# Optimization experiments

Measured on AMD Instinct MI355X. Metric: run time of the kernel, lower is better.

The kernel has to match this reference:

```python
import jax, jax.numpy as jnp
import numpy as np

I, H = 512, 1024

def setup_inputs() -> dict:
    key = jax.random.key(0)
    ks = jax.random.split(key, 5)
    s_ih = 1.0 / np.sqrt(I)
    s_hh = 1.0 / np.sqrt(H)
    return {
        "x": jax.random.normal(ks[0], (512, 64, I), dtype=jnp.float32),
        "W_ih": jax.random.uniform(ks[1], (4 * H, I), minval=-s_ih, maxval=s_ih, dtype=jnp.float32),
        "b_ih": jax.random.uniform(ks[2], (4 * H,), minval=-s_ih, maxval=s_ih, dtype=jnp.float32),
        "W_hh": jax.random.uniform(ks[3], (4 * H, H), minval=-s_hh, maxval=s_hh, dtype=jnp.float32),
        "b_hh": jax.random.uniform(ks[4], (4 * H,), minval=-s_hh, maxval=s_hh, dtype=jnp.float32),
    }

def _lstm(x, W_ih, b_ih, W_hh, b_hh):
    T, B, _ = x.shape
    Hh = W_hh.shape[1]
    # Precompute input projection for all timesteps: [T, B, 4H]
    x_proj = jnp.einsum("tbi,gi->tbg", x, W_ih) + b_ih + b_hh

    def step(carry, xp):
        h, c = carry
        gates = xp + h @ W_hh.T  # [B, 4H]
        i_g, f_g, g_g, o_g = jnp.split(gates, 4, axis=1)
        i_g = jax.nn.sigmoid(i_g)
        f_g = jax.nn.sigmoid(f_g)
        g_g = jnp.tanh(g_g)
        o_g = jax.nn.sigmoid(o_g)
        c = f_g * c + i_g * g_g
        h = o_g * jnp.tanh(c)
        return (h, c), h

    h0 = jnp.zeros((B, Hh), dtype=x.dtype)
    c0 = jnp.zeros((B, Hh), dtype=x.dtype)
    (hT, cT), out = jax.lax.scan(step, (h0, c0), x_proj)
    return out, (hT, cT)

def reference(x, W_ih, b_ih, W_hh, b_hh):
    out, (hT, cT) = _lstm(x, W_ih, b_ih, W_hh, b_hh)
    return out, hT, cT
```

## Files before the change

kernel.cpp:

```cpp
#include <hip/hip_runtime.h>

#define T_STEPS 512
#define BATCH   64
#define IN      512
#define HID     1024
#define GDIM    4096
#define MROWS   (T_STEPS * BATCH)

typedef __attribute__((ext_vector_type(8))) short bf16x8_t;
typedef __attribute__((ext_vector_type(4))) float f32x4_t;

__device__ __forceinline__ unsigned short f2bf(float f) {
  union { float f; unsigned int u; } v; v.f = f;
  unsigned int r = v.u + 0x7FFFu + ((v.u >> 16) & 1u);
  return (unsigned short)(r >> 16);
}
__device__ __forceinline__ float bf2f(unsigned short u) {
  union { unsigned int u; float f; } v; v.u = ((unsigned int)u) << 16;
  return v.f;
}
__device__ __forceinline__ float sigmoidf_(float x) {
  return 1.0f / (1.0f + __expf(-x));
}
__device__ __forceinline__ float tanhf_(float x) {
  return 1.0f - 2.0f / (__expf(2.0f * x) + 1.0f);
}

__global__ void k_cvt(const float* __restrict__ src, unsigned short* __restrict__ dst, int n) {
  int i = (blockIdx.x * blockDim.x + threadIdx.x) * 4;
  if (i + 3 < n) {
    float4 f = *(const float4*)(src + i);
    ushort4 o;
    o.x = f2bf(f.x); o.y = f2bf(f.y); o.z = f2bf(f.z); o.w = f2bf(f.w);
    *(ushort4*)(dst + i) = o;
  }
}

__global__ void k_bias(const float* __restrict__ a, const float* __restrict__ b,
                       float* __restrict__ o) {
  int i = blockIdx.x * blockDim.x + threadIdx.x;
  if (i < GDIM) o[i] = a[i] + b[i];
}

__global__ __launch_bounds__(256) void k_xproj(
    const float* __restrict__ x,
    const unsigned short* __restrict__ Wih,
    const float* __restrict__ bias,
    unsigned short* __restrict__ xproj)
{
  const int AP = 40;
  __shared__ unsigned short Alds[128 * AP];
  __shared__ unsigned short Blds[128 * AP];
  const int tid = threadIdx.x;
  const int w = tid >> 6, l = tid & 63;
  const int m0 = blockIdx.y * 128, n0 = blockIdx.x * 128;
  const int wm = (w >> 1) * 64, wn = (w & 1) * 64;
  f32x4_t acc[4][4] = {};

  for (int k0 = 0; k0 < IN; k0 += 32) {
    #pragma unroll
    for (int it = 0; it < 2; ++it) {
      int chunk = tid + it * 256;
      int row = chunk >> 2;
      int kc  = (chunk & 3) * 8;
      const float* src = x + (size_t)(m0 + row) * IN + k0 + kc;
      float4 f0 = *(const float4*)(src);
      float4 f1 = *(const float4*)(src + 4);
      union { bf16x8_t v; unsigned short s[8]; } u;
      u.s[0]=f2bf(f0.x); u.s[1]=f2bf(f0.y); u.s[2]=f2bf(f0.z); u.s[3]=f2bf(f0.w);
      u.s[4]=f2bf(f1.x); u.s[5]=f2bf(f1.y); u.s[6]=f2bf(f1.z); u.s[7]=f2bf(f1.w);
      *(bf16x8_t*)&Alds[row * AP + kc] = u.v;
    }
    #pragma unroll
    for (int it = 0; it < 2; ++it) {
      int chunk = tid + it * 256;
      int row = chunk >> 2;
      int kc  = (chunk & 3) * 8;
      *(bf16x8_t*)&Blds[row * AP + kc] =
          *(const bf16x8_t*)(Wih + (size_t)(n0 + row) * IN + k0 + kc);
    }
    __syncthreads();
    bf16x8_t a[4], b[4];
    #pragma unroll
    for (int i = 0; i < 4; ++i)
      a[i] = *(const bf16x8_t*)&Alds[(wm + i * 16 + (l & 15)) * AP + ((l >> 4) * 8)];
    #pragma unroll
    for (int i = 0; i < 4; ++i)
      b[i] = *(const bf16x8_t*)&Blds[(wn + i * 16 + (l & 15)) * AP + ((l >> 4) * 8)];
    #pragma unroll
    for (int mi = 0; mi < 4; ++mi) {
      #pragma unroll
      for (int ni = 0; ni < 4; ++ni)
        acc[mi][ni] = __builtin_amdgcn_mfma_f32_16x16x32_bf16(a[mi], b[ni], acc[mi][ni], 0, 0, 0);
    }
    __syncthreads();
  }
  #pragma unroll
  for (int ni = 0; ni < 4; ++ni) {
    int col = n0 + wn + ni * 16 + (l & 15);
    float bv = bias[col];
    #pragma unroll
    for (int mi = 0; mi < 4; ++mi) {
      int rbase = m0 + wm + mi * 16 + (l >> 4) * 4;
      #pragma unroll
      for (int r = 0; r < 4; ++r)
        xproj[(size_t)(rbase + r) * GDIM + col] = f2bf(acc[mi][ni][r] + bv);
    }
  }
}

__global__ __launch_bounds__(256, 1) void k_lstm_persist(
    const unsigned short* __restrict__ xproj,
    const unsigned short* __restrict__ Whh,
    unsigned short* __restrict__ hbuf0,
    unsigned short* __restrict__ hbuf1,
    float* __restrict__ out,
    float* __restrict__ hT,
    float* __restrict__ cT,
    unsigned int* __restrict__ bar)
{
  __shared__ __align__(16) unsigned short Hlds[16384];
  __shared__ float Glds[4][16][17];

  const int tid = threadIdx.x;
  const int w = tid >> 6, l = tid & 63;
  const int bg = blockIdx.x >> 6;
  const int cs = blockIdx.x & 63;
  const int b0 = bg * 16, n0 = cs * 16;

  const int gc = (w << 10) + n0 + (l & 15);
  const unsigned short* wp = Whh + (size_t)gc * HID + ((l >> 4) * 8);
  bf16x8_t wfrag[32];
  #pragma unroll
  for (int ks = 0; ks < 32; ++ks)
    wfrag[ks] = *(const bf16x8_t*)(wp + ks * 32);

  const int eb = tid >> 4, en = tid & 15;
  const size_t ci = (size_t)(b0 + eb) * HID + n0 + en;
  float creg = 0.0f;

  const int abase = (l & 15) * 2048 + ((l >> 4) * 16);
  const int amask = (l & 7) << 4;

  unsigned int* const myflag_base = bar + bg * 512;

  #pragma unroll 1
  for (int t = 0; t < T_STEPS; ++t) {
    const unsigned short* hc = (t & 1) ? hbuf1 : hbuf0;
    unsigned short*       hn = (t & 1) ? hbuf0 : hbuf1;

    const unsigned short* xpp = xproj + ((size_t)t * BATCH + b0 + eb) * GDIM + n0 + en;
    unsigned short x0 = xpp[0], x1 = xpp[1024], x2 = xpp[2048], x3 = xpp[3072];
    asm volatile("" ::: "memory");

    if (t > 0) {
      if (tid == 0) {
        const unsigned int* f = myflag_base + (t - 1);
        while (__hip_atomic_load(f, __ATOMIC_RELAXED, __HIP_MEMORY_SCOPE_AGENT) < 64u)
          __builtin_amdgcn_s_sleep(1);
      }
      __syncthreads();
    }

    {
      const char* hsrc = (const char*)(hc + (size_t)b0 * HID);
      bf16x8_t hv8[8];
      #pragma unroll
      for (int i = 0; i < 8; ++i) {
        unsigned long long ap = (unsigned long long)(hsrc + (size_t)(i * 256 + tid) * 16);
        asm volatile("global_load_dwordx4 %0, %1, off sc0 sc1"
                     : "=v"(hv8[i]) : "v"(ap) : "memory");
      }
      asm volatile("s_waitcnt vmcnt(0)" ::: "memory");
      __builtin_amdgcn_sched_barrier(0);
      #pragma unroll
      for (int i = 0; i < 8; ++i) {
        int d = (i * 256 + tid) * 16;
        int sd = d ^ (((d >> 11) & 7) << 4);
        *(bf16x8_t*)((char*)Hlds + sd) = hv8[i];
      }
    }
    __syncthreads();

    f32x4_t ac0 = {0,0,0,0}, ac1 = {0,0,0,0}, ac2 = {0,0,0,0}, ac3 = {0,0,0,0};
    #pragma unroll
    for (int ks = 0; ks < 32; ks += 4) {
      bf16x8_t a0 = *(const bf16x8_t*)((const char*)Hlds + ((abase + (ks+0)*64) ^ amask));
      bf16x8_t a1 = *(const bf16x8_t*)((const char*)Hlds + ((abase + (ks+1)*64) ^ amask));
      bf16x8_t a2 = *(const bf16x8_t*)((const char*)Hlds + ((abase + (ks+2)*64) ^ amask));
      bf16x8_t a3 = *(const bf16x8_t*)((const char*)Hlds + ((abase + (ks+3)*64) ^ amask));
      ac0 = __builtin_amdgcn_mfma_f32_16x16x32_bf16(a0, wfrag[ks+0], ac0, 0, 0, 0);
      ac1 = __builtin_amdgcn_mfma_f32_16x16x32_bf16(a1, wfrag[ks+1], ac1, 0, 0, 0);
      ac2 = __builtin_amdgcn_mfma_f32_16x16x32_bf16(a2, wfrag[ks+2], ac2, 0, 0, 0);
      ac3 = __builtin_amdgcn_mfma_f32_16x16x32_bf16(a3, wfrag[ks+3], ac3, 0, 0, 0);
    }
    f32x4_t s = ac0 + ac1 + ac2 + ac3;

    {
      int r0 = (l >> 4) * 4, cc = l & 15;
      Glds[w][r0 + 0][cc] = s[0];
      Glds[w][r0 + 1][cc] = s[1];
      Glds[w][r0 + 2][cc] = s[2];
      Glds[w][r0 + 3][cc] = s[3];
    }
    __syncthreads();

    float pre0 = Glds[0][eb][en] + bf2f(x0);
    float pre1 = Glds[1][eb][en] + bf2f(x1);
    float pre2 = Glds[2][eb][en] + bf2f(x2);
    float pre3 = Glds[3][eb][en] + bf2f(x3);
    float ig = sigmoidf_(pre0);
    float fg = sigmoidf_(pre1);
    float gg = tanhf_(pre2);
    float og = sigmoidf_(pre3);
    creg = fg * creg + ig * gg;
    float hv = og * tanhf_(creg);

    out[((size_t)t * BATCH + b0 + eb) * HID + n0 + en] = hv;

    if (t == T_STEPS - 1) {
      hT[ci] = hv;
      cT[ci] = creg;
    } else {
      unsigned short mybf = f2bf(hv);
      unsigned short pbf = (unsigned short)(unsigned int)__shfl_xor((int)(unsigned int)mybf, 1, 64);
      if ((en & 1) == 0) {
        unsigned int pk = ((unsigned int)mybf) | (((unsigned int)pbf) << 16);
        __hip_atomic_store((unsigned int*)(hn + ci), pk,
                           __ATOMIC_RELAXED, __HIP_MEMORY_SCOPE_AGENT);
      }
      asm volatile("s_waitcnt vmcnt(0)" ::: "memory");
      __syncthreads();
      if (tid == 0)
        __hip_atomic_fetch_add(myflag_base + t, 1u,
                               __ATOMIC_RELAXED, __HIP_MEMORY_SCOPE_AGENT);
    }
  }
}

__global__ __launch_bounds__(256) void k_step_fused(
    const unsigned short* __restrict__ hprev,
    unsigned short* __restrict__ hnext,
    float* __restrict__ cstate,
    const unsigned short* __restrict__ Whh,
    const unsigned short* __restrict__ Wih,
    const float* __restrict__ x,
    const float* __restrict__ bias,
    float* __restrict__ out,
    float* __restrict__ hT, float* __restrict__ cT,
    int t, int is_last)
{
  const int RS = 1560;
  const int XB = 1032;
  __shared__ unsigned short Hlds[16 * RS];
  __shared__ float Glds[4][16][17];
  const int tid = threadIdx.x;
  const int w = tid >> 6, l = tid & 63;
  const int bg = blockIdx.x >> 6, hs = blockIdx.x & 63;
  const int b0 = bg * 16, n0 = hs * 16;

  #pragma unroll
  for (int it = 0; it < 8; ++it) {
    int chunk = tid + it * 256;
    int row = chunk >> 7;
    int cc  = (chunk & 127) * 8;
    *(bf16x8_t*)&Hlds[row * RS + cc] =
        *(const bf16x8_t*)(hprev + (size_t)(b0 + row) * HID + cc);
  }
  #pragma unroll
  for (int it = 0; it < 4; ++it) {
    int chunk = tid + it * 256;
    int row = chunk >> 6;
    int cc  = (chunk & 63) * 8;
    const float* src = x + ((size_t)t * BATCH + b0 + row) * IN + cc;
    float4 f0 = *(const float4*)(src);
    float4 f1 = *(const float4*)(src + 4);
    union { bf16x8_t v; unsigned short s[8]; } u;
    u.s[0]=f2bf(f0.x); u.s[1]=f2bf(f0.y); u.s[2]=f2bf(f0.z); u.s[3]=f2bf(f0.w);
    u.s[4]=f2bf(f1.x); u.s[5]=f2bf(f1.y); u.s[6]=f2bf(f1.z); u.s[7]=f2bf(f1.w);
    *(bf16x8_t*)&Hlds[row * RS + XB + cc] = u.v;
  }
  __syncthreads();

  f32x4_t acc = {0.f, 0.f, 0.f, 0.f};
  const int gcol = (w << 10) + n0 + (l & 15);
  const unsigned short* wp = Whh + (size_t)gcol * HID + ((l >> 4) * 8);
  const unsigned short* ap = &Hlds[(l & 15) * RS + ((l >> 4) * 8)];
  #pragma unroll 4
  for (int ks = 0; ks < 32; ++ks) {
    bf16x8_t a = *(const bf16x8_t*)(ap);
    bf16x8_t b = *(const bf16x8_t*)(wp);
    acc = __builtin_amdgcn_mfma_f32_16x16x32_bf16(a, b, acc, 0, 0, 0);
    ap += 32; wp += 32;
  }
  const unsigned short* wpx = Wih + (size_t)gcol * IN + ((l >> 4) * 8);
  const unsigned short* apx = &Hlds[(l & 15) * RS + XB + ((l >> 4) * 8)];
  #pragma unroll 4
  for (int ks = 0; ks < 16; ++ks) {
    bf16x8_t a = *(const bf16x8_t*)(apx);
    bf16x8_t b = *(const bf16x8_t*)(wpx);
    acc = __builtin_amdgcn_mfma_f32_16x16x32_bf16(a, b, acc, 0, 0, 0);
    apx += 32; wpx += 32;
  }

  {
    int r0 = (l >> 4) * 4, cc = l & 15;
    Glds[w][r0 + 0][cc] = acc[0];
    Glds[w][r0 + 1][cc] = acc[1];
    Glds[w][r0 + 2][cc] = acc[2];
    Glds[w][r0 + 3][cc] = acc[3];
  }
  __syncthreads();

  int b = tid >> 4, n = tid & 15;
  float pre[4];
  #pragma unroll
  for (int g = 0; g < 4; ++g)
    pre[g] = Glds[g][b][n] + bias[(g << 10) + n0 + n];
  float ig = sigmoidf_(pre[0]);
  float fg = sigmoidf_(pre[1]);
  float gg = tanhf_(pre[2]);
  float og = sigmoidf_(pre[3]);
  size_t ci = (size_t)(b0 + b) * HID + n0 + n;
  float cn = fg * cstate[ci] + ig * gg;
  float hv = og * tanhf_(cn);
  cstate[ci] = cn;
  out[((size_t)t * BATCH + b0 + b) * HID + n0 + n] = hv;
  hnext[ci] = f2bf(hv);
  if (is_last) { hT[ci] = hv; cT[ci] = cn; }
}

extern "C" void kernel_launch(void* const* d_in, const int* in_sizes, int n_in,
                              void* d_out, int out_size, void* d_ws, size_t ws_size,
                              hipStream_t stream) {
  const float* x    = (const float*)d_in[0];
  const float* Wihf = (const float*)d_in[1];
  const float* bih  = (const float*)d_in[2];
  const float* Whhf = (const float*)d_in[3];
  const float* bhh  = (const float*)d_in[4];
  float* out = (float*)d_out;

  char* ws = (char*)d_ws;
  size_t off = 0;
  auto take = [&](size_t bytes) {
    char* p = ws + off;
    off = (off + bytes + 255) & ~(size_t)255;
    return p;
  };
  unsigned short* wih_b = (unsigned short*)take((size_t)GDIM * IN * 2);
  unsigned short* whh_b = (unsigned short*)take((size_t)GDIM * HID * 2);
  float*          bias  = (float*)take((size_t)GDIM * 4);
  unsigned short* h0    = (unsigned short*)take((size_t)BATCH * HID * 2);
  unsigned short* h1    = (unsigned short*)take((size_t)BATCH * HID * 2);
  float*          cbuf  = (float*)take((size_t)BATCH * HID * 4);
  unsigned int*   bar   = (unsigned int*)take((size_t)T_STEPS * 4 * 4);
  unsigned short* xproj = (unsigned short*)take((size_t)MROWS * GDIM * 2);
  size_t full_need = off;
  const int primary = (ws_size >= full_need) ? 1 : 0;
  (void)in_sizes; (void)n_in; (void)out_size;

  k_cvt<<<(GDIM * IN / 4 + 255) / 256, 256, 0, stream>>>(Wihf, wih_b, GDIM * IN);
  k_cvt<<<(GDIM * HID / 4 + 255) / 256, 256, 0, stream>>>(Whhf, whh_b, GDIM * HID);
  k_bias<<<(GDIM + 255) / 256, 256, 0, stream>>>(bih, bhh, bias);
  (void)hipMemsetAsync(h0, 0, (size_t)BATCH * HID * 2, stream);

  float* hT = out + (size_t)T_STEPS * BATCH * HID;
  float* cT = hT + (size_t)BATCH * HID;

  if (primary) {
    (void)hipMemsetAsync(bar, 0, (size_t)T_STEPS * 4 * 4, stream);
    k_xproj<<<dim3(GDIM / 128, MROWS / 128), 256, 0, stream>>>(x, wih_b, bias, xproj);
    void* args[8];
    void* p_xproj = (void*)xproj; void* p_whh = (void*)whh_b;
    void* p_h0 = (void*)h0;       void* p_h1 = (void*)h1;
    void* p_out = (void*)out;     void* p_hT = (void*)hT;
    void* p_cT = (void*)cT;       void* p_bar = (void*)bar;
    args[0] = &p_xproj; args[1] = &p_whh; args[2] = &p_h0; args[3] = &p_h1;
    args[4] = &p_out;   args[5] = &p_hT;  args[6] = &p_cT; args[7] = &p_bar;
    (void)hipLaunchCooperativeKernel((const void*)k_lstm_persist,
                                     dim3(256), dim3(256), args, 0, stream);
  } else {
    (void)hipMemsetAsync(cbuf, 0, (size_t)BATCH * HID * 4, stream);
    unsigned short* hp = h0;
    unsigned short* hn = h1;
    for (int t = 0; t < T_STEPS; ++t) {
      int last = (t == T_STEPS - 1) ? 1 : 0;
      k_step_fused<<<256, 256, 0, stream>>>(hp, hn, cbuf, whh_b, wih_b, x, bias,
                                            out, hT, cT, t, last);
      unsigned short* tmp = hp; hp = hn; hn = tmp;
    }
  }
}
```

Baseline: 2.083 ms.

## Fuse input projection into persistent LSTM kernel and use per-block flags

Removes the separate x-projection GEMM and its large bf16 workspace. Each persistent block now computes its slice of the next step's input projection right after publishing h, overlapping it with the wait for other blocks. The grid changes from 256 blocks of 256 threads to 128 blocks of 512 threads, so each block owns 32 hidden columns. The atomic counter barrier is replaced by per-block monotonic step flags that a whole wavefront polls with __all. This adds W_ih global reads and MFMA work to the serial recurrence loop, which could lengthen each step if it is not hidden behind the barrier wait.

```diff
diff --git a/kernel.cpp b/kernel.cpp
--- a/kernel.cpp
+++ b/kernel.cpp
@@ -5,7 +5,6 @@
 #define IN      512
 #define HID     1024
 #define GDIM    4096
-#define MROWS   (T_STEPS * BATCH)
 
 typedef __attribute__((ext_vector_type(8))) short bf16x8_t;
 typedef __attribute__((ext_vector_type(4))) float f32x4_t;
@@ -42,142 +41,120 @@
   if (i < GDIM) o[i] = a[i] + b[i];
 }
 
-__global__ __launch_bounds__(256) void k_xproj(
+__global__ __launch_bounds__(512, 1) void k_lstm_persist(
     const float* __restrict__ x,
     const unsigned short* __restrict__ Wih,
-    const float* __restrict__ bias,
-    unsigned short* __restrict__ xproj)
-{
-  const int AP = 40;
-  __shared__ unsigned short Alds[128 * AP];
-  __shared__ unsigned short Blds[128 * AP];
-  const int tid = threadIdx.x;
-  const int w = tid >> 6, l = tid & 63;
-  const int m0 = blockIdx.y * 128, n0 = blockIdx.x * 128;
-  const int wm = (w >> 1) * 64, wn = (w & 1) * 64;
-  f32x4_t acc[4][4] = {};
-
-  for (int k0 = 0; k0 < IN; k0 += 32) {
-    #pragma unroll
-    for (int it = 0; it < 2; ++it) {
-      int chunk = tid + it * 256;
-      int row = chunk >> 2;
-      int kc  = (chunk & 3) * 8;
-      const float* src = x + (size_t)(m0 + row) * IN + k0 + kc;
-      float4 f0 = *(const float4*)(src);
-      float4 f1 = *(const float4*)(src + 4);
-      union { bf16x8_t v; unsigned short s[8]; } u;
-      u.s[0]=f2bf(f0.x); u.s[1]=f2bf(f0.y); u.s[2]=f2bf(f0.z); u.s[3]=f2bf(f0.w);
-      u.s[4]=f2bf(f1.x); u.s[5]=f2bf(f1.y); u.s[6]=f2bf(f1.z); u.s[7]=f2bf(f1.w);
-      *(bf16x8_t*)&Alds[row * AP + kc] = u.v;
-    }
-    #pragma unroll
-    for (int it = 0; it < 2; ++it) {
-      int chunk = tid + it * 256;
-      int row = chunk >> 2;
-      int kc  = (chunk & 3) * 8;
-      *(bf16x8_t*)&Blds[row * AP + kc] =
-          *(const bf16x8_t*)(Wih + (size_t)(n0 + row) * IN + k0 + kc);
-    }
-    __syncthreads();
-    bf16x8_t a[4], b[4];
-    #pragma unroll
-    for (int i = 0; i < 4; ++i)
-      a[i] = *(const bf16x8_t*)&Alds[(wm + i * 16 + (l & 15)) * AP + ((l >> 4) * 8)];
-    #pragma unroll
-    for (int i = 0; i < 4; ++i)
-      b[i] = *(const bf16x8_t*)&Blds[(wn + i * 16 + (l & 15)) * AP + ((l >> 4) * 8)];
-    #pragma unroll
-    for (int mi = 0; mi < 4; ++mi) {
-      #pragma unroll
-      for (int ni = 0; ni < 4; ++ni)
-        acc[mi][ni] = __builtin_amdgcn_mfma_f32_16x16x32_bf16(a[mi], b[ni], acc[mi][ni], 0, 0, 0);
-    }
-    __syncthreads();
-  }
-  #pragma unroll
-  for (int ni = 0; ni < 4; ++ni) {
-    int col = n0 + wn + ni * 16 + (l & 15);
-    float bv = bias[col];
-    #pragma unroll
-    for (int mi = 0; mi < 4; ++mi) {
-      int rbase = m0 + wm + mi * 16 + (l >> 4) * 4;
-      #pragma unroll
-      for (int r = 0; r < 4; ++r)
-        xproj[(size_t)(rbase + r) * GDIM + col] = f2bf(acc[mi][ni][r] + bv);
-    }
-  }
-}
-
-__global__ __launch_bounds__(256, 1) void k_lstm_persist(
-    const unsigned short* __restrict__ xproj,
     const unsigned short* __restrict__ Whh,
+    const float* __restrict__ bih,
+    const float* __restrict__ bhh,
     unsigned short* __restrict__ hbuf0,
     unsigned short* __restrict__ hbuf1,
     float* __restrict__ out,
     float* __restrict__ hT,
     float* __restrict__ cT,
-    unsigned int* __restrict__ bar)
+    unsigned int* __restrict__ flags)
 {
-  __shared__ __align__(16) unsigned short Hlds[16384];
-  __shared__ float Glds[4][16][17];
+  __shared__ __align__(16) unsigned short Hlds[16 * 1024];
+  __shared__ __align__(16) unsigned short Xlds[16 * 512];
+  __shared__ float Glds[4][16][34];
+  __shared__ float XGlds[4][16][34];
 
   const int tid = threadIdx.x;
   const int w = tid >> 6, l = tid & 63;
-  const int bg = blockIdx.x >> 6;
-  const int cs = blockIdx.x & 63;
-  const int b0 = bg * 16, n0 = cs * 16;
-
-  const int gc = (w << 10) + n0 + (l & 15);
+  const int bg  = blockIdx.x >> 5;
+  const int cso = blockIdx.x & 31;
+  const int b0 = bg * 16, n0 = cso * 32;
+  const int g = w & 3, ch = w >> 2;
+  const int gc = (g << 10) + n0 + ch * 16 + (l & 15);
+
   const unsigned short* wp = Whh + (size_t)gc * HID + ((l >> 4) * 8);
   bf16x8_t wfrag[32];
   #pragma unroll
   for (int ks = 0; ks < 32; ++ks)
     wfrag[ks] = *(const bf16x8_t*)(wp + ks * 32);
-
-  const int eb = tid >> 4, en = tid & 15;
+  const unsigned short* wpx = Wih + (size_t)gc * IN + ((l >> 4) * 8);
+
+  const float bv = bih[gc] + bhh[gc];
+
+  const int eb = tid >> 5, en = tid & 31;
   const size_t ci = (size_t)(b0 + eb) * HID + n0 + en;
   float creg = 0.0f;
 
   const int abase = (l & 15) * 2048 + ((l >> 4) * 16);
+  const int xbase = (l & 15) * 1024 + ((l >> 4) * 16);
   const int amask = (l & 7) << 4;
 
-  unsigned int* const myflag_base = bar + bg * 512;
+  unsigned int* const fgrp = flags + bg * 64;
+  unsigned int* const fown = fgrp + cso;
+  const unsigned int* const fpoll = fgrp + (l & 31);
+
+  const int mrow = (l >> 4) * 4, mcc = ch * 16 + (l & 15);
+
+  {
+    const float4* x4 = (const float4*)(x + (size_t)b0 * IN);
+    float4 a0 = x4[2 * tid],          a1 = x4[2 * tid + 1];
+    float4 b0v = x4[2 * (512 + tid)], b1v = x4[2 * (512 + tid) + 1];
+    union { bf16x8_t v; unsigned short s[8]; } u;
+    u.s[0]=f2bf(a0.x); u.s[1]=f2bf(a0.y); u.s[2]=f2bf(a0.z); u.s[3]=f2bf(a0.w);
+    u.s[4]=f2bf(a1.x); u.s[5]=f2bf(a1.y); u.s[6]=f2bf(a1.z); u.s[7]=f2bf(a1.w);
+    { int d = tid * 16; int sd = d ^ (((d >> 10) & 7) << 4);
+      *(bf16x8_t*)((char*)Xlds + sd) = u.v; }
+    u.s[0]=f2bf(b0v.x); u.s[1]=f2bf(b0v.y); u.s[2]=f2bf(b0v.z); u.s[3]=f2bf(b0v.w);
+    u.s[4]=f2bf(b1v.x); u.s[5]=f2bf(b1v.y); u.s[6]=f2bf(b1v.z); u.s[7]=f2bf(b1v.w);
+    { int d = (512 + tid) * 16; int sd = d ^ (((d >> 10) & 7) << 4);
+      *(bf16x8_t*)((char*)Xlds + sd) = u.v; }
+    __syncthreads();
+    f32x4_t sx = {0,0,0,0};
+    #pragma unroll
+    for (int ks = 0; ks < 16; ++ks) {
+      bf16x8_t a = *(const bf16x8_t*)((const char*)Xlds + ((xbase + ks*64) ^ amask));
+      bf16x8_t b = *(const bf16x8_t*)(wpx + ks * 32);
+      sx = __builtin_amdgcn_mfma_f32_16x16x32_bf16(a, b, sx, 0, 0, 0);
+    }
+    XGlds[g][mrow + 0][mcc] = sx[0] + bv;
+    XGlds[g][mrow + 1][mcc] = sx[1] + bv;
+    XGlds[g][mrow + 2][mcc] = sx[2] + bv;
+    XGlds[g][mrow + 3][mcc] = sx[3] + bv;
+  }
 
   #pragma unroll 1
   for (int t = 0; t < T_STEPS; ++t) {
     const unsigned short* hc = (t & 1) ? hbuf1 : hbuf0;
     unsigned short*       hn = (t & 1) ? hbuf0 : hbuf1;
 
-    const unsigned short* xpp = xproj + ((size_t)t * BATCH + b0 + eb) * GDIM + n0 + en;
-    unsigned short x0 = xpp[0], x1 = xpp[1024], x2 = xpp[2048], x3 = xpp[3072];
-    asm volatile("" ::: "memory");
+    float4 xa0, xa1, xb0, xb1;
+    if (t + 1 < T_STEPS) {
+      const float4* x4 = (const float4*)(x + ((size_t)(t + 1) * BATCH + b0) * IN);
+      xa0 = x4[2 * tid];          xa1 = x4[2 * tid + 1];
+      xb0 = x4[2 * (512 + tid)];  xb1 = x4[2 * (512 + tid) + 1];
+      asm volatile("" ::: "memory");
+    }
 
     if (t > 0) {
-      if (tid == 0) {
-        const unsigned int* f = myflag_base + (t - 1);
-        while (__hip_atomic_load(f, __ATOMIC_RELAXED, __HIP_MEMORY_SCOPE_AGENT) < 64u)
-          __builtin_amdgcn_s_sleep(1);
-      }
-      __syncthreads();
+      for (;;) {
+        unsigned int v = __hip_atomic_load(fpoll, __ATOMIC_RELAXED,
+                                           __HIP_MEMORY_SCOPE_AGENT);
+        if (__all((int)(v >= (unsigned int)t))) break;
+        __builtin_amdgcn_s_sleep(1);
+      }
     }
 
     {
       const char* hsrc = (const char*)(hc + (size_t)b0 * HID);
-      bf16x8_t hv8[8];
+      bf16x8_t hv4[4];
       #pragma unroll
-      for (int i = 0; i < 8; ++i) {
-        unsigned long long ap = (unsigned long long)(hsrc + (size_t)(i * 256 + tid) * 16);
+      for (int i = 0; i < 4; ++i) {
+        unsigned long long ap_ = (unsigned long long)(hsrc + (size_t)(i * 512 + tid) * 16);
         asm volatile("global_load_dwordx4 %0, %1, off sc0 sc1"
-                     : "=v"(hv8[i]) : "v"(ap) : "memory");
+                     : "=v"(hv4[i]) : "v"(ap_) : "memory");
       }
       asm volatile("s_waitcnt vmcnt(0)" ::: "memory");
       __builtin_amdgcn_sched_barrier(0);
       #pragma unroll
-      for (int i = 0; i < 8; ++i) {
-        int d = (i * 256 + tid) * 16;
+      for (int i = 0; i < 4; ++i) {
+        int d = (i * 512 + tid) * 16;
         int sd = d ^ (((d >> 11) & 7) << 4);
-        *(bf16x8_t*)((char*)Hlds + sd) = hv8[i];
+        *(bf16x8_t*)((char*)Hlds + sd) = hv4[i];
       }
     }
     __syncthreads();
@@ -195,20 +172,16 @@
       ac3 = __builtin_amdgcn_mfma_f32_16x16x32_bf16(a3, wfrag[ks+3], ac3, 0, 0, 0);
     }
     f32x4_t s = ac0 + ac1 + ac2 + ac3;
-
-    {
-      int r0 = (l >> 4) * 4, cc = l & 15;
-      Glds[w][r0 + 0][cc] = s[0];
-      Glds[w][r0 + 1][cc] = s[1];
-      Glds[w][r0 + 2][cc] = s[2];
-      Glds[w][r0 + 3][cc] = s[3];
-    }
+    Glds[g][mrow + 0][mcc] = s[0];
+    Glds[g][mrow + 1][mcc] = s[1];
+    Glds[g][mrow + 2][mcc] = s[2];
+    Glds[g][mrow + 3][mcc] = s[3];
     __syncthreads();
 
-    float pre0 = Glds[0][eb][en] + bf2f(x0);
-    float pre1 = Glds[1][eb][en] + bf2f(x1);
-    float pre2 = Glds[2][eb][en] + bf2f(x2);
-    float pre3 = Glds[3][eb][en] + bf2f(x3);
+    float pre0 = Glds[0][eb][en] + XGlds[0][eb][en];
+    float pre1 = Glds[1][eb][en] + XGlds[1][eb][en];
+    float pre2 = Glds[2][eb][en] + XGlds[2][eb][en];
+    float pre3 = Glds[3][eb][en] + XGlds[3][eb][en];
     float ig = sigmoidf_(pre0);
     float fg = sigmoidf_(pre1);
     float gg = tanhf_(pre2);
@@ -223,8 +196,9 @@
       cT[ci] = creg;
     } else {
       unsigned short mybf = f2bf(hv);
-      unsigned short pbf = (unsigned short)(unsigned int)__shfl_xor((int)(unsigned int)mybf, 1, 64);
-      if ((en & 1) == 0) {
+      unsigned short pbf = (unsigned short)(unsigned int)
+          __shfl_xor((int)(unsigned int)mybf, 1, 64);
+      if ((l & 1) == 0) {
         unsigned int pk = ((unsigned int)mybf) | (((unsigned int)pbf) << 16);
         __hip_atomic_store((unsigned int*)(hn + ci), pk,
                            __ATOMIC_RELAXED, __HIP_MEMORY_SCOPE_AGENT);
@@ -232,8 +206,30 @@
       asm volatile("s_waitcnt vmcnt(0)" ::: "memory");
       __syncthreads();
       if (tid == 0)
-        __hip_atomic_fetch_add(myflag_base + t, 1u,
-                               __ATOMIC_RELAXED, __HIP_MEMORY_SCOPE_AGENT);
+        __hip_atomic_store(fown, (unsigned int)(t + 1),
+                           __ATOMIC_RELAXED, __HIP_MEMORY_SCOPE_AGENT);
+
+      union { bf16x8_t v; unsigned short s[8]; } u;
+      u.s[0]=f2bf(xa0.x); u.s[1]=f2bf(xa0.y); u.s[2]=f2bf(xa0.z); u.s[3]=f2bf(xa0.w);
+      u.s[4]=f2bf(xa1.x); u.s[5]=f2bf(xa1.y); u.s[6]=f2bf(xa1.z); u.s[7]=f2bf(xa1.w);
+      { int d = tid * 16; int sd = d ^ (((d >> 10) & 7) << 4);
+        *(bf16x8_t*)((char*)Xlds + sd) = u.v; }
+      u.s[0]=f2bf(xb0.x); u.s[1]=f2bf(xb0.y); u.s[2]=f2bf(xb0.z); u.s[3]=f2bf(xb0.w);
+      u.s[4]=f2bf(xb1.x); u.s[5]=f2bf(xb1.y); u.s[6]=f2bf(xb1.z); u.s[7]=f2bf(xb1.w);
+      { int d = (512 + tid) * 16; int sd = d ^ (((d >> 10) & 7) << 4);
+        *(bf16x8_t*)((char*)Xlds + sd) = u.v; }
+      __syncthreads();
+      f32x4_t sx = {0,0,0,0};
+      #pragma unroll
+      for (int ks = 0; ks < 16; ++ks) {
+        bf16x8_t a = *(const bf16x8_t*)((const char*)Xlds + ((xbase + ks*64) ^ amask));
+        bf16x8_t b = *(const bf16x8_t*)(wpx + ks * 32);
+        sx = __builtin_amdgcn_mfma_f32_16x16x32_bf16(a, b, sx, 0, 0, 0);
+      }
+      XGlds[g][mrow + 0][mcc] = sx[0] + bv;
+      XGlds[g][mrow + 1][mcc] = sx[1] + bv;
+      XGlds[g][mrow + 2][mcc] = sx[2] + bv;
+      XGlds[g][mrow + 3][mcc] = sx[3] + bv;
     }
   }
 }
@@ -353,33 +349,32 @@
   unsigned short* h0    = (unsigned short*)take((size_t)BATCH * HID * 2);
   unsigned short* h1    = (unsigned short*)take((size_t)BATCH * HID * 2);
   float*          cbuf  = (float*)take((size_t)BATCH * HID * 4);
-  unsigned int*   bar   = (unsigned int*)take((size_t)T_STEPS * 4 * 4);
-  unsigned short* xproj = (unsigned short*)take((size_t)MROWS * GDIM * 2);
+  unsigned int*   flags = (unsigned int*)take((size_t)4 * 64 * 4);
   size_t full_need = off;
   const int primary = (ws_size >= full_need) ? 1 : 0;
   (void)in_sizes; (void)n_in; (void)out_size;
 
   k_cvt<<<(GDIM * IN / 4 + 255) / 256, 256, 0, stream>>>(Wihf, wih_b, GDIM * IN);
   k_cvt<<<(GDIM * HID / 4 + 255) / 256, 256, 0, stream>>>(Whhf, whh_b, GDIM * HID);
-  k_bias<<<(GDIM + 255) / 256, 256, 0, stream>>>(bih, bhh, bias);
   (void)hipMemsetAsync(h0, 0, (size_t)BATCH * HID * 2, stream);
 
   float* hT = out + (size_t)T_STEPS * BATCH * HID;
   float* cT = hT + (size_t)BATCH * HID;
 
   if (primary) {
-    (void)hipMemsetAsync(bar, 0, (size_t)T_STEPS * 4 * 4, stream);
-    k_xproj<<<dim3(GDIM / 128, MROWS / 128), 256, 0, stream>>>(x, wih_b, bias, xproj);
-    void* args[8];
-    void* p_xproj = (void*)xproj; void* p_whh = (void*)whh_b;
-    void* p_h0 = (void*)h0;       void* p_h1 = (void*)h1;
-    void* p_out = (void*)out;     void* p_hT = (void*)hT;
-    void* p_cT = (void*)cT;       void* p_bar = (void*)bar;
-    args[0] = &p_xproj; args[1] = &p_whh; args[2] = &p_h0; args[3] = &p_h1;
-    args[4] = &p_out;   args[5] = &p_hT;  args[6] = &p_cT; args[7] = &p_bar;
+    (void)hipMemsetAsync(flags, 0, (size_t)4 * 64 * 4, stream);
+    void* p_x = (void*)x;       void* p_wih = (void*)wih_b;
+    void* p_whh = (void*)whh_b; void* p_bih = (void*)bih;
+    void* p_bhh = (void*)bhh;   void* p_h0 = (void*)h0;
+    void* p_h1 = (void*)h1;     void* p_out = (void*)out;
+    void* p_hT = (void*)hT;     void* p_cT = (void*)cT;
+    void* p_fl = (void*)flags;
+    void* args[11] = {&p_x, &p_wih, &p_whh, &p_bih, &p_bhh, &p_h0, &p_h1,
+                      &p_out, &p_hT, &p_cT, &p_fl};
     (void)hipLaunchCooperativeKernel((const void*)k_lstm_persist,
-                                     dim3(256), dim3(256), args, 0, stream);
+                                     dim3(128), dim3(512), args, 0, stream);
   } else {
+    k_bias<<<(GDIM + 255) / 256, 256, 0, stream>>>(bih, bhh, bias);
     (void)hipMemsetAsync(cbuf, 0, (size_t)BATCH * HID * 4, stream);
     unsigned short* hp = h0;
     unsigned short* hn = h1;
```

New measurement: 3.419 ms. 1.64x slower.

## Replace per-block atomic counter barrier with per-wave monotonic flags polled by each wave

Applied to the files above, without the earlier changes.

Swaps the per-step group barrier, where thread 0 spins on an atomic counter and the block then runs __syncthreads, for per-wave flags that store the step number. Every wave polls all 256 flags of its batch group with one vector load per lane and proceeds once all are at least t. This drops the block-wide __syncthreads and the atomic fetch-add from the critical path of each timestep. It also adds an empty asm constraint so the W_hh fragments stay pinned in registers. The cost is more polling traffic, since every wave now reads 1 KB of flags per spin, and correctness relies on per-wave ordering of the h stores before each flag store.

```diff
diff --git a/kernel.cpp b/kernel.cpp
--- a/kernel.cpp
+++ b/kernel.cpp
@@ -9,6 +9,7 @@
 
 typedef __attribute__((ext_vector_type(8))) short bf16x8_t;
 typedef __attribute__((ext_vector_type(4))) float f32x4_t;
+typedef __attribute__((ext_vector_type(4))) unsigned int u32x4_t;
 
 __device__ __forceinline__ unsigned short f2bf(float f) {
   union { float f; unsigned int u; } v; v.f = f;
@@ -117,7 +118,7 @@
     float* __restrict__ out,
     float* __restrict__ hT,
     float* __restrict__ cT,
-    unsigned int* __restrict__ bar)
+    unsigned int* __restrict__ flags)
 {
   __shared__ __align__(16) unsigned short Hlds[16384];
   __shared__ float Glds[4][16][17];
@@ -134,6 +135,9 @@
   #pragma unroll
   for (int ks = 0; ks < 32; ++ks)
     wfrag[ks] = *(const bf16x8_t*)(wp + ks * 32);
+  #pragma unroll
+  for (int ks = 0; ks < 32; ++ks)
+    asm volatile("" : "+v"(wfrag[ks]));
 
   const int eb = tid >> 4, en = tid & 15;
   const size_t ci = (size_t)(b0 + eb) * HID + n0 + en;
@@ -142,7 +146,9 @@
   const int abase = (l & 15) * 2048 + ((l >> 4) * 16);
   const int amask = (l & 7) << 4;
 
-  unsigned int* const myflag_base = bar + bg * 512;
+  unsigned int* const fgrp = flags + bg * 256;
+  unsigned int* const fown = fgrp + cs * 4 + w;
+  const unsigned long long fap = (unsigned long long)(fgrp + l * 4);
 
   #pragma unroll 1
   for (int t = 0; t < T_STEPS; ++t) {
@@ -154,12 +160,16 @@
     asm volatile("" ::: "memory");
 
     if (t > 0) {
-      if (tid == 0) {
-        const unsigned int* f = myflag_base + (t - 1);
-        while (__hip_atomic_load(f, __ATOMIC_RELAXED, __HIP_MEMORY_SCOPE_AGENT) < 64u)
-          __builtin_amdgcn_s_sleep(1);
+      const unsigned int tu = (unsigned int)t;
+      for (;;) {
+        u32x4_t v;
+        asm volatile("global_load_dwordx4 %0, %1, off sc0 sc1"
+                     : "=v"(v) : "v"(fap) : "memory");
+        asm volatile("s_waitcnt vmcnt(0)" ::: "memory");
+        int ok = (v[0] >= tu) & (v[1] >= tu) & (v[2] >= tu) & (v[3] >= tu);
+        if (__all(ok)) break;
+        __builtin_amdgcn_s_sleep(1);
       }
-      __syncthreads();
     }
 
     {
@@ -223,17 +233,17 @@
       cT[ci] = creg;
     } else {
       unsigned short mybf = f2bf(hv);
-      unsigned short pbf = (unsigned short)(unsigned int)__shfl_xor((int)(unsigned int)mybf, 1, 64);
-      if ((en & 1) == 0) {
+      unsigned short pbf = (unsigned short)(unsigned int)
+          __shfl_xor((int)(unsigned int)mybf, 1, 64);
+      if ((l & 1) == 0) {
         unsigned int pk = ((unsigned int)mybf) | (((unsigned int)pbf) << 16);
         __hip_atomic_store((unsigned int*)(hn + ci), pk,
                            __ATOMIC_RELAXED, __HIP_MEMORY_SCOPE_AGENT);
       }
       asm volatile("s_waitcnt vmcnt(0)" ::: "memory");
-      __syncthreads();
-      if (tid == 0)
-        __hip_atomic_fetch_add(myflag_base + t, 1u,
-                               __ATOMIC_RELAXED, __HIP_MEMORY_SCOPE_AGENT);
+      if (l == 0)
+        __hip_atomic_store(fown, (unsigned int)(t + 1),
+                           __ATOMIC_RELAXED, __HIP_MEMORY_SCOPE_AGENT);
     }
   }
 }
@@ -353,7 +363,7 @@
   unsigned short* h0    = (unsigned short*)take((size_t)BATCH * HID * 2);
   unsigned short* h1    = (unsigned short*)take((size_t)BATCH * HID * 2);
   float*          cbuf  = (float*)take((size_t)BATCH * HID * 4);
-  unsigned int*   bar   = (unsigned int*)take((size_t)T_STEPS * 4 * 4);
+  unsigned int*   flags = (unsigned int*)take((size_t)4 * 256 * 4);
   unsigned short* xproj = (unsigned short*)take((size_t)MROWS * GDIM * 2);
   size_t full_need = off;
   const int primary = (ws_size >= full_need) ? 1 : 0;
@@ -368,15 +378,13 @@
   float* cT = hT + (size_t)BATCH * HID;
 
   if (primary) {
-    (void)hipMemsetAsync(bar, 0, (size_t)T_STEPS * 4 * 4, stream);
+    (void)hipMemsetAsync(flags, 0, (size_t)4 * 256 * 4, stream);
     k_xproj<<<dim3(GDIM / 128, MROWS / 128), 256, 0, stream>>>(x, wih_b, bias, xproj);
-    void* args[8];
     void* p_xproj = (void*)xproj; void* p_whh = (void*)whh_b;
     void* p_h0 = (void*)h0;       void* p_h1 = (void*)h1;
     void* p_out = (void*)out;     void* p_hT = (void*)hT;
-    void* p_cT = (void*)cT;       void* p_bar = (void*)bar;
-    args[0] = &p_xproj; args[1] = &p_whh; args[2] = &p_h0; args[3] = &p_h1;
-    args[4] = &p_out;   args[5] = &p_hT;  args[6] = &p_cT; args[7] = &p_bar;
+    void* p_cT = (void*)cT;       void* p_fl = (void*)flags;
+    void* args[8] = {&p_xproj, &p_whh, &p_h0, &p_h1, &p_out, &p_hT, &p_cT, &p_fl};
     (void)hipLaunchCooperativeKernel((const void*)k_lstm_persist,
                                      dim3(256), dim3(256), args, 0, stream);
   } else {
```

After: 3.797 ms. 1.82x slower.

## Retile persistent LSTM blocks to 8x32 so fewer blocks share each barrier

Applied to the files above, without the earlier changes.

Each persistent block now computes 8 batch rows by 32 hidden columns instead of 16x16. Each block issues two MFMA column tiles and keeps twice the W_hh fragments in registers. Each barrier group shrinks from 64 to 32 blocks, and each block reads half as much h per step. The cost is that half of each 16-row MFMA is wasted on zero-padded rows, and register pressure rises. The output store is also moved after the flag signal so it leaves the critical path, and a fallback runs if the cooperative launch fails.

```diff
diff --git a/kernel.cpp b/kernel.cpp
--- a/kernel.cpp
+++ b/kernel.cpp
@@ -24,6 +24,9 @@
 }
 __device__ __forceinline__ float tanhf_(float x) {
   return 1.0f - 2.0f / (__expf(2.0f * x) + 1.0f);
+}
+__device__ __forceinline__ f32x4_t MFMA_(bf16x8_t a, bf16x8_t b, f32x4_t c) {
+  return __builtin_amdgcn_mfma_f32_16x16x32_bf16(a, b, c, 0, 0, 0);
 }
 
 __global__ void k_cvt(const float* __restrict__ src, unsigned short* __restrict__ dst, int n) {
@@ -120,29 +123,42 @@
     unsigned int* __restrict__ bar)
 {
   __shared__ __align__(16) unsigned short Hlds[16384];
-  __shared__ float Glds[4][16][17];
+  __shared__ float Glds[4][8][33];
 
   const int tid = threadIdx.x;
   const int w = tid >> 6, l = tid & 63;
-  const int bg = blockIdx.x >> 6;
-  const int cs = blockIdx.x & 63;
-  const int b0 = bg * 16, n0 = cs * 16;
-
-  const int gc = (w << 10) + n0 + (l & 15);
-  const unsigned short* wp = Whh + (size_t)gc * HID + ((l >> 4) * 8);
-  bf16x8_t wfrag[32];
-  #pragma unroll
-  for (int ks = 0; ks < 32; ++ks)
-    wfrag[ks] = *(const bf16x8_t*)(wp + ks * 32);
-
-  const int eb = tid >> 4, en = tid & 15;
+  const int grp  = blockIdx.x >> 5;
+  const int slot = blockIdx.x & 31;
+  const int b0 = grp * 8, n0 = slot * 32;
+
+  {
+    bf16x8_t zv = {0, 0, 0, 0, 0, 0, 0, 0};
+    #pragma unroll
+    for (int i = 0; i < 8; ++i)
+      *(bf16x8_t*)((char*)Hlds + (size_t)(i * 256 + tid) * 16) = zv;
+  }
+  __syncthreads();
+
+  bf16x8_t wf[64];
+  {
+    const unsigned short* wp0 =
+        Whh + (size_t)((w << 10) + n0 + (l & 15)) * HID + ((l >> 4) * 8);
+    const unsigned short* wp1 = wp0 + (size_t)16 * HID;
+    #pragma unroll
+    for (int ks = 0; ks < 32; ++ks) {
+      wf[ks]      = *(const bf16x8_t*)(wp0 + ks * 32);
+      wf[32 + ks] = *(const bf16x8_t*)(wp1 + ks * 32);
+    }
+  }
+
+  const int eb = tid >> 5, en = tid & 31;
   const size_t ci = (size_t)(b0 + eb) * HID + n0 + en;
   float creg = 0.0f;
 
   const int abase = (l & 15) * 2048 + ((l >> 4) * 16);
   const int amask = (l & 7) << 4;
 
-  unsigned int* const myflag_base = bar + bg * 512;
+  unsigned int* const fgrp = bar + grp * 512;
 
   #pragma unroll 1
   for (int t = 0; t < T_STEPS; ++t) {
@@ -155,8 +171,8 @@
 
     if (t > 0) {
       if (tid == 0) {
-        const unsigned int* f = myflag_base + (t - 1);
-        while (__hip_atomic_load(f, __ATOMIC_RELAXED, __HIP_MEMORY_SCOPE_AGENT) < 64u)
+        const unsigned int* f = fgrp + (t - 1);
+        while (__hip_atomic_load(f, __ATOMIC_RELAXED, __HIP_MEMORY_SCOPE_AGENT) < 32u)
           __builtin_amdgcn_s_sleep(1);
       }
       __syncthreads();
@@ -164,44 +180,44 @@
 
     {
       const char* hsrc = (const char*)(hc + (size_t)b0 * HID);
-      bf16x8_t hv8[8];
+      bf16x8_t hv[4];
       #pragma unroll
-      for (int i = 0; i < 8; ++i) {
+      for (int i = 0; i < 4; ++i) {
         unsigned long long ap = (unsigned long long)(hsrc + (size_t)(i * 256 + tid) * 16);
         asm volatile("global_load_dwordx4 %0, %1, off sc0 sc1"
-                     : "=v"(hv8[i]) : "v"(ap) : "memory");
+                     : "=v"(hv[i]) : "v"(ap) : "memory");
       }
       asm volatile("s_waitcnt vmcnt(0)" ::: "memory");
       __builtin_amdgcn_sched_barrier(0);
       #pragma unroll
-      for (int i = 0; i < 8; ++i) {
+      for (int i = 0; i < 4; ++i) {
         int d = (i * 256 + tid) * 16;
         int sd = d ^ (((d >> 11) & 7) << 4);
-        *(bf16x8_t*)((char*)Hlds + sd) = hv8[i];
+        *(bf16x8_t*)((char*)Hlds + sd) = hv[i];
       }
     }
     __syncthreads();
 
     f32x4_t ac0 = {0,0,0,0}, ac1 = {0,0,0,0}, ac2 = {0,0,0,0}, ac3 = {0,0,0,0};
     #pragma unroll
-    for (int ks = 0; ks < 32; ks += 4) {
+    for (int ks = 0; ks < 32; ks += 2) {
       bf16x8_t a0 = *(const bf16x8_t*)((const char*)Hlds + ((abase + (ks+0)*64) ^ amask));
       bf16x8_t a1 = *(const bf16x8_t*)((const char*)Hlds + ((abase + (ks+1)*64) ^ amask));
-      bf16x8_t a2 = *(const bf16x8_t*)((const char*)Hlds + ((abase + (ks+2)*64) ^ amask));
-      bf16x8_t a3 = *(const bf16x8_t*)((const char*)Hlds + ((abase + (ks+3)*64) ^ amask));
-      ac0 = __builtin_amdgcn_mfma_f32_16x16x32_bf16(a0, wfrag[ks+0], ac0, 0, 0, 0);
-      ac1 = __builtin_amdgcn_mfma_f32_16x16x32_bf16(a1, wfrag[ks+1], ac1, 0, 0, 0);
-      ac2 = __builtin_amdgcn_mfma_f32_16x16x32_bf16(a2, wfrag[ks+2], ac2, 0, 0, 0);
-      ac3 = __builtin_amdgcn_mfma_f32_16x16x32_bf16(a3, wfrag[ks+3], ac3, 0, 0, 0);
-    }
-    f32x4_t s = ac0 + ac1 + ac2 + ac3;
-
-    {
+      ac0 = MFMA_(a0, wf[ks],          ac0);
+      ac1 = MFMA_(a0, wf[32 + ks],     ac1);
+      ac2 = MFMA_(a1, wf[ks + 1],      ac2);
+      ac3 = MFMA_(a1, wf[32 + ks + 1], ac3);
+    }
+    f32x4_t s0 = ac0 + ac2;
+    f32x4_t s1 = ac1 + ac3;
+
+    if ((l >> 4) < 2) {
       int r0 = (l >> 4) * 4, cc = l & 15;
-      Glds[w][r0 + 0][cc] = s[0];
-      Glds[w][r0 + 1][cc] = s[1];
-      Glds[w][r0 + 2][cc] = s[2];
-      Glds[w][r0 + 3][cc] = s[3];
+      #pragma unroll
+      for (int j = 0; j < 4; ++j) {
+        Glds[w][r0 + j][cc]      = s0[j];
+        Glds[w][r0 + j][16 + cc] = s1[j];
+      }
     }
     __syncthreads();
 
@@ -216,15 +232,15 @@
     creg = fg * creg + ig * gg;
     float hv = og * tanhf_(creg);
 
-    out[((size_t)t * BATCH + b0 + eb) * HID + n0 + en] = hv;
-
     if (t == T_STEPS - 1) {
+      out[((size_t)t * BATCH + b0 + eb) * HID + n0 + en] = hv;
       hT[ci] = hv;
       cT[ci] = creg;
     } else {
       unsigned short mybf = f2bf(hv);
-      unsigned short pbf = (unsigned short)(unsigned int)__shfl_xor((int)(unsigned int)mybf, 1, 64);
-      if ((en & 1) == 0) {
+      unsigned short pbf = (unsigned short)(unsigned int)
+          __shfl_xor((int)(unsigned int)mybf, 1, 64);
+      if ((l & 1) == 0) {
         unsigned int pk = ((unsigned int)mybf) | (((unsigned int)pbf) << 16);
         __hip_atomic_store((unsigned int*)(hn + ci), pk,
                            __ATOMIC_RELAXED, __HIP_MEMORY_SCOPE_AGENT);
@@ -232,8 +248,9 @@
       asm volatile("s_waitcnt vmcnt(0)" ::: "memory");
       __syncthreads();
       if (tid == 0)
-        __hip_atomic_fetch_add(myflag_base + t, 1u,
-                               __ATOMIC_RELAXED, __HIP_MEMORY_SCOPE_AGENT);
+        (void)__hip_atomic_fetch_add(fgrp + t, 1u,
+                                     __ATOMIC_RELAXED, __HIP_MEMORY_SCOPE_AGENT);
+      out[((size_t)t * BATCH + b0 + eb) * HID + n0 + en] = hv;
     }
   }
 }
@@ -353,7 +370,7 @@
   unsigned short* h0    = (unsigned short*)take((size_t)BATCH * HID * 2);
   unsigned short* h1    = (unsigned short*)take((size_t)BATCH * HID * 2);
   float*          cbuf  = (float*)take((size_t)BATCH * HID * 4);
-  unsigned int*   bar   = (unsigned int*)take((size_t)T_STEPS * 4 * 4);
+  unsigned int*   bar   = (unsigned int*)take((size_t)8 * 512 * 4);
   unsigned short* xproj = (unsigned short*)take((size_t)MROWS * GDIM * 2);
   size_t full_need = off;
   const int primary = (ws_size >= full_need) ? 1 : 0;
@@ -368,26 +385,25 @@
   float* cT = hT + (size_t)BATCH * HID;
 
   if (primary) {
-    (void)hipMemsetAsync(bar, 0, (size_t)T_STEPS * 4 * 4, stream);
+    (void)hipMemsetAsync(bar, 0, (size_t)8 * 512 * 4, stream);
     k_xproj<<<dim3(GDIM / 128, MROWS / 128), 256, 0, stream>>>(x, wih_b, bias, xproj);
-    void* args[8];
     void* p_xproj = (void*)xproj; void* p_whh = (void*)whh_b;
     void* p_h0 = (void*)h0;       void* p_h1 = (void*)h1;
     void* p_out = (void*)out;     void* p_hT = (void*)hT;
-    void* p_cT = (void*)cT;       void* p_bar = (void*)bar;
-    args[0] = &p_xproj; args[1] = &p_whh; args[2] = &p_h0; args[3] = &p_h1;
-    args[4] = &p_out;   args[5] = &p_hT;  args[6] = &p_cT; args[7] = &p_bar;
-    (void)hipLaunchCooperativeKernel((const void*)k_lstm_persist,
-                                     dim3(256), dim3(256), args, 0, stream);
-  } else {
-    (void)hipMemsetAsync(cbuf, 0, (size_t)BATCH * HID * 4, stream);
-    unsigned short* hp = h0;
-    unsigned short* hn = h1;
-    for (int t = 0; t < T_STEPS; ++t) {
-      int last = (t == T_STEPS - 1) ? 1 : 0;
-      k_step_fused<<<256, 256, 0, stream>>>(hp, hn, cbuf, whh_b, wih_b, x, bias,
-                                            out, hT, cT, t, last);
-      unsigned short* tmp = hp; hp = hn; hn = tmp;
-    }
-  }
-}
+    void* p_cT = (void*)cT;       void* p_fl = (void*)bar;
+    void* args[8] = {&p_xproj, &p_whh, &p_h0, &p_h1, &p_out, &p_hT, &p_cT, &p_fl};
+    hipError_t err = hipLaunchCooperativeKernel((const void*)k_lstm_persist,
+                                                dim3(256), dim3(256), args, 0, stream);
+    if (err == hipSuccess) return;
+  }
+
+  (void)hipMemsetAsync(cbuf, 0, (size_t)BATCH * HID * 4, stream);
+  unsigned short* hp = h0;
+  unsigned short* hn = h1;
+  for (int t = 0; t < T_STEPS; ++t) {
+    int last = (t == T_STEPS - 1) ? 1 : 0;
+    k_step_fused<<<256, 256, 0, stream>>>(hp, hn, cbuf, whh_b, wih_b, x, bias,
+                                          out, hT, cT, t, last);
+    unsigned short* tmp = hp; hp = hn; hn = tmp;
+  }
+}
```

After: 2.041 ms. 2.0% less time.
